# Optimization experiments

Measured on AMD Instinct MI355X. Metric: run time of the kernel, lower is better.

Reference implementation:

```python
import jax, jax.numpy as jnp
import numpy as np

N_Q = 10           # qubits
N_BLOCKS = 10      # encoding blocks (== N_Q so adjoint start-index arithmetic matches source)
DIM = 1 << N_Q     # 1024 state-vector dimension
P = 128            # number of data points -> P*P pairwise circuit evaluations

SQRT2 = np.float32(np.sqrt(2.0))

# bits[d, q] = q-th bit (MSB-first) of basis index d
_bits_np = ((np.arange(DIM)[:, None] >> (N_Q - 1 - np.arange(N_Q))) & 1).astype(np.float32)
BITS = jnp.asarray(_bits_np)  # [DIM, N_Q]
# CRZ-ring diagonal feature: control q, target (q+1) % N_Q; phase exp(1j*theta_q*s_q*(s_{q+1}-1/2))
RING = jnp.asarray(_bits_np * (np.roll(_bits_np, -1, axis=1) - 0.5))  # [DIM, N_Q]


def _apply_1q(state, U, q):
    # state: [B, DIM]; apply 2x2 U to qubit q (MSB-first ordering)
    B = state.shape[0]
    s = state.reshape(B, 1 << q, 2, 1 << (N_Q - q - 1))
    s = jnp.einsum('ij,bajc->baic', U, s)
    return s.reshape(B, DIM)


def h_layer(state):
    H = jnp.asarray([[1, 1], [1, -1]], dtype=state.dtype) / SQRT2
    for q in range(N_Q):
        state = _apply_1q(state, H, q)
    return state


def rz_layer(state, thetas):
    # thetas: [B, N_Q] per-pair data angles; RZ(t) = diag(e^{-it/2}, e^{it/2})
    phases = jnp.exp(1j * jnp.einsum('dq,bq->bd', BITS - 0.5, thetas))
    return state * phases.astype(state.dtype)


def ry_layer(state, thetas):
    # thetas: [N_Q] shared trainable angles
    for q in range(N_Q):
        c, s = jnp.cos(thetas[q] / 2), jnp.sin(thetas[q] / 2)
        U = jnp.stack([jnp.stack([c, -s]), jnp.stack([s, c])]).astype(state.dtype)
        state = _apply_1q(state, U, q)
    return state


def crz_ring(state, thetas):
    # entire CRZ ring is diagonal in the computational basis -> single fused multiply
    phases = jnp.exp(1j * (RING @ thetas))  # [DIM]
    return state * phases.astype(state.dtype)


def circuit(x1, x2, params):
    # x1, x2: [B, N_BLOCKS*N_Q]; params: [N_BLOCKS, 2, N_Q]
    B = x1.shape[0]
    state = jnp.zeros((B, DIM), jnp.complex64).at[:, 0].set(1.0)
    for j in range(N_BLOCKS):  # block(...)
        state = h_layer(state)
        state = rz_layer(state, x1[:, j * N_Q:(j + 1) * N_Q])
        state = ry_layer(state, params[j, 0])
        state = crz_ring(state, params[j, 1])
    for k in range(N_BLOCKS):  # adj_block(...) over reversed(params)
        bp = params[N_BLOCKS - 1 - k]
        start = (N_Q - k - 1) * N_Q  # exactly as written in the source
        state = crz_ring(state, -bp[1])   # adjoint of diagonal gate = negated angles
        state = ry_layer(state, -bp[0])   # RY(-t); single-qubit gates commute across qubits
        state = rz_layer(state, -x2[:, start:start + N_Q])
        state = h_layer(state)            # H is self-adjoint
    return state


def setup_inputs() -> dict:
    key = jax.random.key(0)
    k1, k2, k3 = jax.random.split(key, 3)
    data = jax.random.normal(k1, (P, N_BLOCKS * N_Q), jnp.float32)
    labels = jnp.sign(jax.random.normal(k2, (P,), jnp.float32))  # +/-1 class labels
    params = jax.random.normal(k3, (N_BLOCKS, 2, N_Q), jnp.float32)
    return {"data": data, "labels": labels, "params": params}


def reference(data, labels, params):
    # k_fusion: kernel-target-alignment over all (i, j) pairs, fully batched
    n = data.shape[0]
    x1 = jnp.repeat(data, n, axis=0)   # point i for each pair (pair-major)
    x2 = jnp.tile(data, (n, 1))        # point j for each pair
    state = circuit(x1, x2, params)
    K = (jnp.abs(state[:, 0]) ** 2).reshape(n, n)  # probability of |0...0>
    ll = labels[:, None] * labels[None, :]
    polarity = jnp.sum(ll * K)
    norm = jnp.sqrt(jnp.sum(K ** 2) * jnp.sum(ll ** 2))
    return polarity / norm
```

## Files before the change

kernel.cpp:

```cpp
#include <hip/hip_runtime.h>
#include <math.h>

#define NQ   10
#define DIM  1024
#define NB   10
#define NPTS 128
#define S2   0.70710678118654752440f

#define TS 32
#define KC 64
#define KSPLIT (DIM / KC)
#define NBLK_RED 64

typedef float f2 __attribute__((ext_vector_type(2)));

__device__ __forceinline__ f2 cmul(f2 a, f2 b) {
    return (f2){a.x * b.x - a.y * b.y, a.x * b.y + a.y * b.x};
}

__global__ __launch_bounds__(256)
void states_kernel(const float* __restrict__ data,
                   const float* __restrict__ params,
                   float2* __restrict__ psi,
                   double* __restrict__ acc,
                   int* __restrict__ cnt)
{
    __shared__ f2    Tb[2][16 * 64];
    __shared__ f2    UT[NB * NQ * 4];
    __shared__ float sCrz[NB * NQ];

    const int tid  = threadIdx.x;
    const int w    = tid >> 6;
    const int lane = tid & 63;
    const int pt   = blockIdx.x;

    if (pt == 0 && tid == 0) { acc[0] = 0.0; acc[1] = 0.0; cnt[0] = 0; }

    if (tid < NB * NQ) {
        const int j = tid / NQ, q = tid - j * NQ;
        const float th = params[j * 2 * NQ + q];
        float c, s;
        __sincosf(0.5f * th, &s, &c);
        const float x = data[pt * (NB * NQ) + tid];
        float cx, sx;
        __sincosf(0.5f * x, &sx, &cx);
        const float al = (c - s) * S2, be = (c + s) * S2;
        f2* u = &UT[tid * 4];
        u[0] = (f2){ al * cx, -be * sx};
        u[1] = (f2){ be * cx, -al * sx};
        u[2] = (f2){ be * cx,  al * sx};
        u[3] = (f2){-al * cx, -be * sx};
        sCrz[tid] = params[j * 2 * NQ + NQ + q];
    }
    __syncthreads();

    f2 v[4];
    #pragma unroll
    for (int m = 0; m < 4; ++m) v[m] = (f2){0.f, 0.f};
    if (tid == 0) v[0] = (f2){1.f, 0.f};

    const float B2 = (float)( lane       & 1), B3 = (float)((lane >> 1) & 1);
    const float B4 = (float)((lane >> 2) & 1), B5 = (float)((lane >> 3) & 1);
    const float B6 = (float)((lane >> 4) & 1), B7 = (float)((lane >> 5) & 1);

    #define LOAD_U(j, q) \
        const f2* _u = &UT[((j) * NQ + (q)) * 4]; \
        const f2 u0 = _u[0], u1 = _u[1], u2 = _u[2], u3 = _u[3];

    #define APPLY_LOCAL(j, q, bit) { \
        LOAD_U(j, q) \
        _Pragma("unroll") \
        for (int m = 0; m < 4; ++m) if (!(m & (bit))) { \
            const f2 a0 = v[m], a1 = v[m | (bit)]; \
            v[m]         = cmul(u0, a0) + cmul(u1, a1); \
            v[m | (bit)] = cmul(u2, a0) + cmul(u3, a1); \
        } }

    #define APPLY_SHUFFLE(j, q, mb) { \
        LOAD_U(j, q) \
        const bool hi = lane & (mb); \
        const f2 cv = hi ? u3 : u0; \
        const f2 cp = hi ? u2 : u1; \
        _Pragma("unroll") \
        for (int m = 0; m < 4; ++m) { \
            const f2 p = { __shfl_xor(v[m].x, (mb), 64), \
                           __shfl_xor(v[m].y, (mb), 64) }; \
            v[m] = cmul(cv, v[m]) + cmul(cp, p); \
        } }

    #define TRANSPOSE(buf) { \
        f2* T = Tb[buf]; \
        _Pragma("unroll") \
        for (int m = 0; m < 4; ++m) T[(w * 4 + m) * 64 + lane] = v[m]; \
        __syncthreads(); \
        f2 nv0 = T[(0 * 4 + w) * 64 + lane]; \
        f2 nv1 = T[(1 * 4 + w) * 64 + lane]; \
        f2 nv2 = T[(2 * 4 + w) * 64 + lane]; \
        f2 nv3 = T[(3 * 4 + w) * 64 + lane]; \
        v[0] = nv0; v[1] = nv1; v[2] = nv2; v[3] = nv3; }

    #define APPLY_CRZ(j, hiIsAmp) { \
        const float* phi = &sCrz[(j) * NQ]; \
        const float laneOnly = phi[2] * B7 * (B6 - 0.5f) \
                             + phi[3] * B6 * (B5 - 0.5f) \
                             + phi[4] * B5 * (B4 - 0.5f) \
                             + phi[5] * B4 * (B3 - 0.5f) \
                             + phi[6] * B3 * (B2 - 0.5f); \
        _Pragma("unroll") \
        for (int m = 0; m < 4; ++m) { \
            const int hi2 = (hiIsAmp) ? m : w; \
            const int lo2 = (hiIsAmp) ? w : m; \
            const float b9 = (float)((hi2 >> 1) & 1), b8 = (float)(hi2 & 1); \
            const float b1 = (float)((lo2 >> 1) & 1), b0 = (float)(lo2 & 1); \
            const float ph = laneOnly \
                           + phi[0] * b9 * (b8 - 0.5f) \
                           + phi[1] * b8 * (B7 - 0.5f) \
                           + phi[7] * B2 * (b1 - 0.5f) \
                           + phi[8] * b1 * (b0 - 0.5f) \
                           + phi[9] * b0 * (b9 - 0.5f); \
            float sc, cc; \
            __sincosf(ph, &sc, &cc); \
            v[m] = cmul(v[m], (f2){cc, sc}); \
        } }

    #pragma unroll
    for (int jj = 0; jj < NB / 2; ++jj) {
        const int je = 2 * jj;
        APPLY_LOCAL(je, 9, 1)
        APPLY_LOCAL(je, 8, 2)
        APPLY_SHUFFLE(je, 7, 1)
        APPLY_SHUFFLE(je, 6, 2)
        APPLY_SHUFFLE(je, 5, 4)
        APPLY_SHUFFLE(je, 4, 8)
        APPLY_SHUFFLE(je, 3, 16)
        APPLY_SHUFFLE(je, 2, 32)
        TRANSPOSE(0)
        APPLY_LOCAL(je, 1, 1)
        APPLY_LOCAL(je, 0, 2)
        APPLY_CRZ(je, true)

        const int jo = je + 1;
        APPLY_LOCAL(jo, 1, 1)
        APPLY_LOCAL(jo, 0, 2)
        APPLY_SHUFFLE(jo, 7, 1)
        APPLY_SHUFFLE(jo, 6, 2)
        APPLY_SHUFFLE(jo, 5, 4)
        APPLY_SHUFFLE(jo, 4, 8)
        APPLY_SHUFFLE(jo, 3, 16)
        APPLY_SHUFFLE(jo, 2, 32)
        TRANSPOSE(1)
        APPLY_LOCAL(jo, 9, 1)
        APPLY_LOCAL(jo, 8, 2)
        APPLY_CRZ(jo, false)
    }

    float2* o = psi + (size_t)pt * DIM + w * 256 + lane * 4;
    *(float4*)&o[0] = make_float4(v[0].x, v[0].y, v[1].x, v[1].y);
    *(float4*)&o[2] = make_float4(v[2].x, v[2].y, v[3].x, v[3].y);
}

__global__ __launch_bounds__(256)
void gram_kernel(const float2* __restrict__ psi, float2* __restrict__ Gpart)
{
    __shared__ float2 A [TS][KC + 2];
    __shared__ float2 Bt[KC][TS + 2];

    const int tid  = threadIdx.x;
    const int bx   = blockIdx.x;
    const int ks   = bx & 15;
    const int tile = bx >> 4;
    const int ti   = tile >> 2, tj = tile & 3;
    const int kbase = ks * KC;

    #pragma unroll
    for (int it = 0; it < 2; ++it) {
        const int slot = it * 256 + tid;
        const int row  = slot >> 4;
        const int kq   = (slot & 15) << 2;
        const float4* sa = (const float4*)(psi + (ti * TS + row) * DIM + kbase + kq);
        const float4 a01 = sa[0], a23 = sa[1];
        *(float4*)&A[row][kq]     = a01;
        *(float4*)&A[row][kq + 2] = a23;
        const float4* sb = (const float4*)(psi + (tj * TS + row) * DIM + kbase + kq);
        const float4 b01 = sb[0], b23 = sb[1];
        Bt[kq + 0][row] = make_float2(b01.x, b01.y);
        Bt[kq + 1][row] = make_float2(b01.z, b01.w);
        Bt[kq + 2][row] = make_float2(b23.x, b23.y);
        Bt[kq + 3][row] = make_float2(b23.z, b23.w);
    }
    __syncthreads();

    const int ty = tid >> 4, tx = tid & 15;
    float g00r = 0.f, g00i = 0.f, g01r = 0.f, g01i = 0.f;
    float g10r = 0.f, g10i = 0.f, g11r = 0.f, g11i = 0.f;

    #pragma unroll 4
    for (int k = 0; k < KC; k += 2) {
        const float4 a0 = *(const float4*)&A[2 * ty    ][k];
        const float4 a1 = *(const float4*)&A[2 * ty + 1][k];
        const float4 b0 = *(const float4*)&Bt[k    ][2 * tx];
        const float4 b1 = *(const float4*)&Bt[k + 1][2 * tx];
        g00r += a0.x * b0.x + a0.y * b0.y;  g00i += a0.x * b0.y - a0.y * b0.x;
        g01r += a0.x * b0.z + a0.y * b0.w;  g01i += a0.x * b0.w - a0.y * b0.z;
        g10r += a1.x * b0.x + a1.y * b0.y;  g10i += a1.x * b0.y - a1.y * b0.x;
        g11r += a1.x * b0.z + a1.y * b0.w;  g11i += a1.x * b0.w - a1.y * b0.z;
        g00r += a0.z * b1.x + a0.w * b1.y;  g00i += a0.z * b1.y - a0.w * b1.x;
        g01r += a0.z * b1.z + a0.w * b1.w;  g01i += a0.z * b1.w - a0.w * b1.z;
        g10r += a1.z * b1.x + a1.w * b1.y;  g10i += a1.z * b1.y - a1.w * b1.x;
        g11r += a1.z * b1.z + a1.w * b1.w;  g11i += a1.z * b1.w - a1.w * b1.z;
    }

    float2* gp = Gpart + ks * (NPTS * NPTS);
    const int gr0 = ti * TS + 2 * ty, gc0 = tj * TS + 2 * tx;
    gp[(gr0    ) * NPTS + gc0    ] = make_float2(g00r, g00i);
    gp[(gr0    ) * NPTS + gc0 + 1] = make_float2(g01r, g01i);
    gp[(gr0 + 1) * NPTS + gc0    ] = make_float2(g10r, g10i);
    gp[(gr0 + 1) * NPTS + gc0 + 1] = make_float2(g11r, g11i);
}

__global__ __launch_bounds__(256)
void reduce_final(const float2* __restrict__ Gpart,
                  const float* __restrict__ labels,
                  double* __restrict__ acc,
                  int* __restrict__ cnt,
                  float* __restrict__ out)
{
    const int idx = blockIdx.x * 256 + threadIdx.x;
    float gr = 0.f, gi = 0.f;
    #pragma unroll
    for (int p = 0; p < KSPLIT; ++p) {
        const float2 g = Gpart[p * (NPTS * NPTS) + idx];
        gr += g.x; gi += g.y;
    }
    const int i  = idx >> 7;
    const int jj = idx & (NPTS - 1);
    const float K = gr * gr + gi * gi;
    double pol = (double)(labels[i] * labels[jj]) * (double)K;
    double k2  = (double)K * (double)K;
    #pragma unroll
    for (int off = 1; off < 64; off <<= 1) {
        pol += __shfl_xor(pol, off, 64);
        k2  += __shfl_xor(k2,  off, 64);
    }
    __shared__ double sp[4], sk[4];
    const int wv = threadIdx.x >> 6;
    if ((threadIdx.x & 63) == 0) { sp[wv] = pol; sk[wv] = k2; }
    __syncthreads();
    if (threadIdx.x == 0) {
        atomicAdd(&acc[0], sp[0] + sp[1] + sp[2] + sp[3]);
        atomicAdd(&acc[1], sk[0] + sk[1] + sk[2] + sk[3]);
        __threadfence();
        const int done = atomicAdd(cnt, 1);
        if (done == NBLK_RED - 1) {
            const double p  = atomicAdd(&acc[0], 0.0);
            const double s2 = atomicAdd(&acc[1], 0.0);
            double sumL2 = 0.0;
            for (int t = 0; t < NPTS; ++t) {
                const double l = (double)labels[t];
                sumL2 += l * l;
            }
            out[0] = (float)(p / (sumL2 * sqrt(s2)));
        }
    }
}

extern "C" void kernel_launch(void* const* d_in, const int* in_sizes, int n_in,
                              void* d_out, int out_size, void* d_ws, size_t ws_size,
                              hipStream_t stream)
{
    const float* data   = (const float*)d_in[0];
    const float* labels = (const float*)d_in[1];
    const float* params = (const float*)d_in[2];
    float* out = (float*)d_out;

    float2* psi   = (float2*)d_ws;
    float2* Gpart = (float2*)((char*)d_ws + (size_t)(1u << 20));
    double* acc   = (double*)((char*)d_ws + (size_t)(3u << 20));
    int*    cnt   = (int*)   ((char*)d_ws + (size_t)(3u << 20) + 16);

    states_kernel<<<NPTS, 256, 0, stream>>>(data, params, psi, acc, cnt);
    gram_kernel<<<256, 256, 0, stream>>>(psi, Gpart);
    reduce_final<<<NBLK_RED, 256, 0, stream>>>(Gpart, labels, acc, cnt, out);
}
```

Before: 88.42 us.

## Fuse qubit-pair gates into 4x4 tables and precompute CRZ phase tables

Combines pairs of single-qubit gates into 4x4 Kronecker matrices, which halves the number of local and shuffle gate passes. Each shuffle pass now does three xor-shuffles per amplitude. CRZ phases are split into a lane-only table and a register/warp table, both computed once per block in shared memory with sincos, so the inner loop no longer evaluates sincos. The first block starts from an analytic product state, which skips applying gates to the basis vector. In exchange it adds shared-memory table setup, more shuffles per pass and more shared-memory reads per gate.

Measured after the change: 87.68 us. About the same (-0.8%).

```diff
diff --git a/kernel.cpp b/kernel.cpp
--- a/kernel.cpp
+++ b/kernel.cpp
@@ -27,6 +27,10 @@
 {
     __shared__ f2    Tb[2][16 * 64];
     __shared__ f2    UT[NB * NQ * 4];
+    __shared__ f2    Kt[NB * 2 * 16];
+    __shared__ f2    Ct[NB * 3 * 16];
+    __shared__ f2    Gt[NB * 64];
+    __shared__ f2    Lt[NB * 64];
     __shared__ float sCrz[NB * NQ];
 
     const int tid  = threadIdx.x;
@@ -38,12 +42,10 @@
 
     if (tid < NB * NQ) {
         const int j = tid / NQ, q = tid - j * NQ;
-        const float th = params[j * 2 * NQ + q];
         float c, s;
-        __sincosf(0.5f * th, &s, &c);
-        const float x = data[pt * (NB * NQ) + tid];
+        __sincosf(0.5f * params[j * 2 * NQ + q], &s, &c);
         float cx, sx;
-        __sincosf(0.5f * x, &sx, &cx);
+        __sincosf(0.5f * data[pt * (NB * NQ) + tid], &sx, &cx);
         const float al = (c - s) * S2, be = (c + s) * S2;
         f2* u = &UT[tid * 4];
         u[0] = (f2){ al * cx, -be * sx};
@@ -54,38 +56,77 @@
     }
     __syncthreads();
 
-    f2 v[4];
-    #pragma unroll
-    for (int m = 0; m < 4; ++m) v[m] = (f2){0.f, 0.f};
-    if (tid == 0) v[0] = (f2){1.f, 0.f};
-
-    const float B2 = (float)( lane       & 1), B3 = (float)((lane >> 1) & 1);
-    const float B4 = (float)((lane >> 2) & 1), B5 = (float)((lane >> 3) & 1);
-    const float B6 = (float)((lane >> 4) & 1), B7 = (float)((lane >> 5) & 1);
-
-    #define LOAD_U(j, q) \
-        const f2* _u = &UT[((j) * NQ + (q)) * 4]; \
-        const f2 u0 = _u[0], u1 = _u[1], u2 = _u[2], u3 = _u[3];
-
-    #define APPLY_LOCAL(j, q, bit) { \
-        LOAD_U(j, q) \
-        _Pragma("unroll") \
-        for (int m = 0; m < 4; ++m) if (!(m & (bit))) { \
-            const f2 a0 = v[m], a1 = v[m | (bit)]; \
-            v[m]         = cmul(u0, a0) + cmul(u1, a1); \
-            v[m | (bit)] = cmul(u2, a0) + cmul(u3, a1); \
-        } }
-
-    #define APPLY_SHUFFLE(j, q, mb) { \
-        LOAD_U(j, q) \
-        const bool hi = lane & (mb); \
-        const f2 cv = hi ? u3 : u0; \
-        const f2 cp = hi ? u2 : u1; \
+    for (int e = tid; e < NB * 2 * 16; e += 256) {
+        const int j = e >> 5, side = (e >> 4) & 1, a = (e >> 2) & 3, b = e & 3;
+        const int qh = side ? 0 : 8, ql = side ? 1 : 9;
+        Kt[e] = cmul(UT[(j * NQ + qh) * 4 + ((a >> 1) * 2 + (b >> 1))],
+                     UT[(j * NQ + ql) * 4 + ((a & 1) * 2 + (b & 1))]);
+    }
+    for (int e = tid; e < NB * 3 * 16; e += 256) {
+        const int j = e / 48, r = e - j * 48;
+        const int p = r >> 4, k = r & 15, combo = k >> 2, t = k & 3;
+        const int la = combo & 1, lb = (combo >> 1) & 1;
+        const int ta = t & 1, tb = (t >> 1) & 1;
+        const int qa = 7 - 2 * p, qb = 6 - 2 * p;
+        Ct[e] = cmul(UT[(j * NQ + qa) * 4 + (la * 2 + (la ^ ta))],
+                     UT[(j * NQ + qb) * 4 + (lb * 2 + (lb ^ tb))]);
+    }
+    for (int e = tid; e < NB * 64; e += 256) {
+        const int j = e >> 6, r = e & 63;
+        const float m1 = (float)((r >> 5) & 1), m0 = (float)((r >> 4) & 1);
+        const float w1 = (float)((r >> 3) & 1), w0 = (float)((r >> 2) & 1);
+        const float b7 = (float)((r >> 1) & 1), b2 = (float)(r & 1);
+        const float* phi = &sCrz[j * NQ];
+        float g;
+        if ((j & 1) == 0)
+            g = phi[0] * m1 * (m0 - 0.5f) + phi[1] * m0 * (b7 - 0.5f)
+              + phi[7] * b2 * (w1 - 0.5f) + phi[8] * w1 * (w0 - 0.5f)
+              + phi[9] * w0 * (m1 - 0.5f);
+        else
+            g = phi[0] * w1 * (w0 - 0.5f) + phi[1] * w0 * (b7 - 0.5f)
+              + phi[7] * b2 * (m1 - 0.5f) + phi[8] * m1 * (m0 - 0.5f)
+              + phi[9] * m0 * (w1 - 0.5f);
+        float s, c;
+        __sincosf(g, &s, &c);
+        Gt[e] = (f2){c, s};
+    }
+    for (int e = tid; e < NB * 64; e += 256) {
+        const int j = e >> 6, ln = e & 63;
+        const float B2 = (float)( ln       & 1), B3 = (float)((ln >> 1) & 1);
+        const float B4 = (float)((ln >> 2) & 1), B5 = (float)((ln >> 3) & 1);
+        const float B6 = (float)((ln >> 4) & 1), B7 = (float)((ln >> 5) & 1);
+        const float* phi = &sCrz[j * NQ];
+        const float lo = phi[2] * B7 * (B6 - 0.5f) + phi[3] * B6 * (B5 - 0.5f)
+                       + phi[4] * B5 * (B4 - 0.5f) + phi[5] * B4 * (B3 - 0.5f)
+                       + phi[6] * B3 * (B2 - 0.5f);
+        float s, c;
+        __sincosf(lo, &s, &c);
+        Lt[e] = (f2){c, s};
+    }
+    __syncthreads();
+
+    const int b72 = ((((lane >> 5) & 1)) << 1) | (lane & 1);
+
+    #define LOCAL4(j, side) { \
+        const f2* Km = &Kt[((j) * 2 + (side)) * 16]; \
+        f2 n0 = cmul(Km[ 0], v[0]) + cmul(Km[ 1], v[1]) + cmul(Km[ 2], v[2]) + cmul(Km[ 3], v[3]); \
+        f2 n1 = cmul(Km[ 4], v[0]) + cmul(Km[ 5], v[1]) + cmul(Km[ 6], v[2]) + cmul(Km[ 7], v[3]); \
+        f2 n2 = cmul(Km[ 8], v[0]) + cmul(Km[ 9], v[1]) + cmul(Km[10], v[2]) + cmul(Km[11], v[3]); \
+        f2 n3 = cmul(Km[12], v[0]) + cmul(Km[13], v[1]) + cmul(Km[14], v[2]) + cmul(Km[15], v[3]); \
+        v[0] = n0; v[1] = n1; v[2] = n2; v[3] = n3; }
+
+    #define SHUF4(j, p) { \
+        const int sh = 2 * (p); \
+        const int combo = (((lane >> (sh + 1)) & 1) << 1) | ((lane >> sh) & 1); \
+        const f2* Cm = &Ct[((j) * 3 + (p)) * 16 + combo * 4]; \
+        const f2 c0 = Cm[0], c1 = Cm[1], c2 = Cm[2], c3 = Cm[3]; \
         _Pragma("unroll") \
         for (int m = 0; m < 4; ++m) { \
-            const f2 p = { __shfl_xor(v[m].x, (mb), 64), \
-                           __shfl_xor(v[m].y, (mb), 64) }; \
-            v[m] = cmul(cv, v[m]) + cmul(cp, p); \
+            const f2 x = v[m]; \
+            const f2 p1 = { __shfl_xor(x.x, 1 << sh, 64), __shfl_xor(x.y, 1 << sh, 64) }; \
+            const f2 p2 = { __shfl_xor(x.x, 2 << sh, 64), __shfl_xor(x.y, 2 << sh, 64) }; \
+            const f2 p3 = { __shfl_xor(x.x, 3 << sh, 64), __shfl_xor(x.y, 3 << sh, 64) }; \
+            v[m] = cmul(c0, x) + cmul(c1, p1) + cmul(c2, p2) + cmul(c3, p3); \
         } }
 
     #define TRANSPOSE(buf) { \
@@ -99,59 +140,44 @@
         f2 nv3 = T[(3 * 4 + w) * 64 + lane]; \
         v[0] = nv0; v[1] = nv1; v[2] = nv2; v[3] = nv3; }
 
-    #define APPLY_CRZ(j, hiIsAmp) { \
-        const float* phi = &sCrz[(j) * NQ]; \
-        const float laneOnly = phi[2] * B7 * (B6 - 0.5f) \
-                             + phi[3] * B6 * (B5 - 0.5f) \
-                             + phi[4] * B5 * (B4 - 0.5f) \
-                             + phi[5] * B4 * (B3 - 0.5f) \
-                             + phi[6] * B3 * (B2 - 0.5f); \
+    #define CRZ4(j) { \
+        const f2 l = Lt[((j) << 6) | lane]; \
         _Pragma("unroll") \
         for (int m = 0; m < 4; ++m) { \
-            const int hi2 = (hiIsAmp) ? m : w; \
-            const int lo2 = (hiIsAmp) ? w : m; \
-            const float b9 = (float)((hi2 >> 1) & 1), b8 = (float)(hi2 & 1); \
-            const float b1 = (float)((lo2 >> 1) & 1), b0 = (float)(lo2 & 1); \
-            const float ph = laneOnly \
-                           + phi[0] * b9 * (b8 - 0.5f) \
-                           + phi[1] * b8 * (B7 - 0.5f) \
-                           + phi[7] * B2 * (b1 - 0.5f) \
-                           + phi[8] * b1 * (b0 - 0.5f) \
-                           + phi[9] * b0 * (b9 - 0.5f); \
-            float sc, cc; \
-            __sincosf(ph, &sc, &cc); \
-            v[m] = cmul(v[m], (f2){cc, sc}); \
+            const f2 g = Gt[((j) << 6) | (m << 4) | (w << 2) | b72]; \
+            v[m] = cmul(v[m], cmul(l, g)); \
         } }
 
+    f2 v[4];
+    {
+        f2 f = UT[2 * 4 + ((lane >> 5) & 1) * 2];
+        #pragma unroll
+        for (int q = 3; q <= 7; ++q)
+            f = cmul(f, UT[q * 4 + ((lane >> (7 - q)) & 1) * 2]);
+        f = cmul(f, UT[8 * 4 + ((w >> 1) & 1) * 2]);
+        f = cmul(f, UT[9 * 4 + (w & 1) * 2]);
+        #pragma unroll
+        for (int m = 0; m < 4; ++m)
+            v[m] = cmul(cmul(UT[0 * 4 + ((m >> 1) & 1) * 2],
+                             UT[1 * 4 + (m & 1) * 2]), f);
+    }
+    CRZ4(0)
+
     #pragma unroll
-    for (int jj = 0; jj < NB / 2; ++jj) {
-        const int je = 2 * jj;
-        APPLY_LOCAL(je, 9, 1)
-        APPLY_LOCAL(je, 8, 2)
-        APPLY_SHUFFLE(je, 7, 1)
-        APPLY_SHUFFLE(je, 6, 2)
-        APPLY_SHUFFLE(je, 5, 4)
-        APPLY_SHUFFLE(je, 4, 8)
-        APPLY_SHUFFLE(je, 3, 16)
-        APPLY_SHUFFLE(je, 2, 32)
-        TRANSPOSE(0)
-        APPLY_LOCAL(je, 1, 1)
-        APPLY_LOCAL(je, 0, 2)
-        APPLY_CRZ(je, true)
-
-        const int jo = je + 1;
-        APPLY_LOCAL(jo, 1, 1)
-        APPLY_LOCAL(jo, 0, 2)
-        APPLY_SHUFFLE(jo, 7, 1)
-        APPLY_SHUFFLE(jo, 6, 2)
-        APPLY_SHUFFLE(jo, 5, 4)
-        APPLY_SHUFFLE(jo, 4, 8)
-        APPLY_SHUFFLE(jo, 3, 16)
-        APPLY_SHUFFLE(jo, 2, 32)
-        TRANSPOSE(1)
-        APPLY_LOCAL(jo, 9, 1)
-        APPLY_LOCAL(jo, 8, 2)
-        APPLY_CRZ(jo, false)
+    for (int j = 1; j < NB; ++j) {
+        if (j & 1) {
+            LOCAL4(j, 1)
+            SHUF4(j, 0) SHUF4(j, 1) SHUF4(j, 2)
+            TRANSPOSE(j & 1)
+            LOCAL4(j, 0)
+            CRZ4(j)
+        } else {
+            LOCAL4(j, 0)
+            SHUF4(j, 0) SHUF4(j, 1) SHUF4(j, 2)
+            TRANSPOSE(j & 1)
+            LOCAL4(j, 1)
+            CRZ4(j)
+        }
     }
 
     float2* o = psi + (size_t)pt * DIM + w * 256 + lane * 4;
```

## Run state simulation with one wavefront per point and shared-memory transposes

Applied to the files above, without the earlier changes.

The states kernel now uses a single 64-lane wavefront per data point, with each lane holding 16 amplitudes. Gates are applied in registers and qubit remapping goes through padded LDS transposes instead of cross-lane shuffles and block-wide barriers. The first block's state is built directly as a product state, and the CRZ phases are precomputed as separable lane and register tables, so the inner loop needs no sincos. The trade-off is higher register pressure and only 128 wavefronts across the whole GPU. The transposes also rely on single-wavefront execution without explicit barriers.

Result: slower. 106.3 us (+20.2%).

```diff
diff --git a/kernel.cpp b/kernel.cpp
--- a/kernel.cpp
+++ b/kernel.cpp
@@ -18,145 +18,145 @@
     return (f2){a.x * b.x - a.y * b.y, a.x * b.y + a.y * b.x};
 }
 
-__global__ __launch_bounds__(256)
+__global__ __launch_bounds__(64)
 void states_kernel(const float* __restrict__ data,
                    const float* __restrict__ params,
                    float2* __restrict__ psi,
                    double* __restrict__ acc,
                    int* __restrict__ cnt)
 {
-    __shared__ f2    Tb[2][16 * 64];
+    __shared__ f2    T[16 * 65];
     __shared__ f2    UT[NB * NQ * 4];
+    __shared__ f2    Lt[NB * 64];
+    __shared__ f2    Gt[NB * 64];
     __shared__ float sCrz[NB * NQ];
 
-    const int tid  = threadIdx.x;
-    const int w    = tid >> 6;
-    const int lane = tid & 63;
+    const int lane = threadIdx.x;
     const int pt   = blockIdx.x;
 
-    if (pt == 0 && tid == 0) { acc[0] = 0.0; acc[1] = 0.0; cnt[0] = 0; }
-
-    if (tid < NB * NQ) {
-        const int j = tid / NQ, q = tid - j * NQ;
-        const float th = params[j * 2 * NQ + q];
+    if (pt == 0 && lane == 0) { acc[0] = 0.0; acc[1] = 0.0; cnt[0] = 0; }
+
+    for (int e = lane; e < NB * NQ; e += 64) {
+        const int j = e / NQ, q = e - j * NQ;
         float c, s;
-        __sincosf(0.5f * th, &s, &c);
-        const float x = data[pt * (NB * NQ) + tid];
+        __sincosf(0.5f * params[j * 2 * NQ + q], &s, &c);
         float cx, sx;
-        __sincosf(0.5f * x, &sx, &cx);
+        __sincosf(0.5f * data[pt * (NB * NQ) + e], &sx, &cx);
         const float al = (c - s) * S2, be = (c + s) * S2;
-        f2* u = &UT[tid * 4];
+        f2* u = &UT[e * 4];
         u[0] = (f2){ al * cx, -be * sx};
         u[1] = (f2){ be * cx, -al * sx};
         u[2] = (f2){ be * cx,  al * sx};
         u[3] = (f2){-al * cx, -be * sx};
-        sCrz[tid] = params[j * 2 * NQ + NQ + q];
-    }
-    __syncthreads();
-
-    f2 v[4];
-    #pragma unroll
-    for (int m = 0; m < 4; ++m) v[m] = (f2){0.f, 0.f};
-    if (tid == 0) v[0] = (f2){1.f, 0.f};
-
-    const float B2 = (float)( lane       & 1), B3 = (float)((lane >> 1) & 1);
-    const float B4 = (float)((lane >> 2) & 1), B5 = (float)((lane >> 3) & 1);
-    const float B6 = (float)((lane >> 4) & 1), B7 = (float)((lane >> 5) & 1);
-
-    #define LOAD_U(j, q) \
+        sCrz[e] = params[j * 2 * NQ + NQ + q];
+    }
+    for (int e = lane; e < NB * 64; e += 64) {
+        const int j = e >> 6, r = e & 63;
+        const float* phi = &sCrz[j * NQ];
+        const float r0 = (float)(r & 1),        r1 = (float)((r >> 1) & 1);
+        const float r2 = (float)((r >> 2) & 1), r3 = (float)((r >> 3) & 1);
+        const float r4 = (float)((r >> 4) & 1), r5 = (float)((r >> 5) & 1);
+        const float m0 = r2, m1 = r3, m2 = r4, m3 = r5;
+        const float bA = r1, bB = r0;
+        float L, G;
+        if ((j & 1) == 0) {
+            L = phi[4] * r5 * (r4 - 0.5f) + phi[5] * r4 * (r3 - 0.5f)
+              + phi[6] * r3 * (r2 - 0.5f) + phi[7] * r2 * (r1 - 0.5f)
+              + phi[8] * r1 * (r0 - 0.5f);
+            G = phi[0] * m3 * (m2 - 0.5f) + phi[1] * m2 * (m1 - 0.5f)
+              + phi[2] * m1 * (m0 - 0.5f) + phi[3] * m0 * (bA - 0.5f)
+              + phi[9] * bB * (m3 - 0.5f);
+        } else {
+            L = phi[0] * r5 * (r4 - 0.5f) + phi[1] * r4 * (r3 - 0.5f)
+              + phi[2] * r3 * (r2 - 0.5f) + phi[3] * r2 * (r1 - 0.5f)
+              + phi[4] * r1 * (r0 - 0.5f);
+            G = phi[6] * m3 * (m2 - 0.5f) + phi[7] * m2 * (m1 - 0.5f)
+              + phi[8] * m1 * (m0 - 0.5f) + phi[5] * bA * (m3 - 0.5f)
+              + phi[9] * m0 * (bB - 0.5f);
+        }
+        float s, c;
+        __sincosf(L, &s, &c);  Lt[e] = (f2){c, s};
+        __sincosf(G, &s, &c);  Gt[e] = (f2){c, s};
+    }
+
+    #define APPLY(j, q, bit) { \
         const f2* _u = &UT[((j) * NQ + (q)) * 4]; \
-        const f2 u0 = _u[0], u1 = _u[1], u2 = _u[2], u3 = _u[3];
-
-    #define APPLY_LOCAL(j, q, bit) { \
-        LOAD_U(j, q) \
-        _Pragma("unroll") \
-        for (int m = 0; m < 4; ++m) if (!(m & (bit))) { \
+        const f2 u0 = _u[0], u1 = _u[1], u2 = _u[2], u3 = _u[3]; \
+        _Pragma("unroll") \
+        for (int m = 0; m < 16; ++m) if (!(m & (bit))) { \
             const f2 a0 = v[m], a1 = v[m | (bit)]; \
             v[m]         = cmul(u0, a0) + cmul(u1, a1); \
             v[m | (bit)] = cmul(u2, a0) + cmul(u3, a1); \
         } }
 
-    #define APPLY_SHUFFLE(j, q, mb) { \
-        LOAD_U(j, q) \
-        const bool hi = lane & (mb); \
-        const f2 cv = hi ? u3 : u0; \
-        const f2 cp = hi ? u2 : u1; \
-        _Pragma("unroll") \
-        for (int m = 0; m < 4; ++m) { \
-            const f2 p = { __shfl_xor(v[m].x, (mb), 64), \
-                           __shfl_xor(v[m].y, (mb), 64) }; \
-            v[m] = cmul(cv, v[m]) + cmul(cp, p); \
+    #define TWRITE() { \
+        _Pragma("unroll") \
+        for (int m = 0; m < 16; ++m) T[m * 65 + lane] = v[m]; }
+
+    #define READ_AD() { \
+        const int base = 65 * (lane & 15) + ((lane >> 4) << 4); \
+        _Pragma("unroll") \
+        for (int m = 0; m < 16; ++m) v[m] = T[base + m]; }
+
+    #define READ_B() { \
+        _Pragma("unroll") \
+        for (int m = 0; m < 16; ++m) \
+            v[m] = T[65 * (((m & 3) << 2) | (lane >> 4)) + ((m >> 2) << 4) + (lane & 15)]; }
+
+    #define READ_C() { \
+        _Pragma("unroll") \
+        for (int m = 0; m < 16; ++m) \
+            v[m] = T[65 * (((lane >> 4) << 2) | (m >> 2)) + ((m & 3) << 4) + (lane & 15)]; }
+
+    #define CRZ(j, crossIdx) { \
+        const f2 l = Lt[((j) << 6) | lane]; \
+        _Pragma("unroll") \
+        for (int m = 0; m < 16; ++m) { \
+            const f2 g = Gt[((j) << 6) | (m << 2) | (crossIdx)]; \
+            v[m] = cmul(v[m], cmul(l, g)); \
         } }
 
-    #define TRANSPOSE(buf) { \
-        f2* T = Tb[buf]; \
-        _Pragma("unroll") \
-        for (int m = 0; m < 4; ++m) T[(w * 4 + m) * 64 + lane] = v[m]; \
-        __syncthreads(); \
-        f2 nv0 = T[(0 * 4 + w) * 64 + lane]; \
-        f2 nv1 = T[(1 * 4 + w) * 64 + lane]; \
-        f2 nv2 = T[(2 * 4 + w) * 64 + lane]; \
-        f2 nv3 = T[(3 * 4 + w) * 64 + lane]; \
-        v[0] = nv0; v[1] = nv1; v[2] = nv2; v[3] = nv3; }
-
-    #define APPLY_CRZ(j, hiIsAmp) { \
-        const float* phi = &sCrz[(j) * NQ]; \
-        const float laneOnly = phi[2] * B7 * (B6 - 0.5f) \
-                             + phi[3] * B6 * (B5 - 0.5f) \
-                             + phi[4] * B5 * (B4 - 0.5f) \
-                             + phi[5] * B4 * (B3 - 0.5f) \
-                             + phi[6] * B3 * (B2 - 0.5f); \
-        _Pragma("unroll") \
-        for (int m = 0; m < 4; ++m) { \
-            const int hi2 = (hiIsAmp) ? m : w; \
-            const int lo2 = (hiIsAmp) ? w : m; \
-            const float b9 = (float)((hi2 >> 1) & 1), b8 = (float)(hi2 & 1); \
-            const float b1 = (float)((lo2 >> 1) & 1), b0 = (float)(lo2 & 1); \
-            const float ph = laneOnly \
-                           + phi[0] * b9 * (b8 - 0.5f) \
-                           + phi[1] * b8 * (B7 - 0.5f) \
-                           + phi[7] * B2 * (b1 - 0.5f) \
-                           + phi[8] * b1 * (b0 - 0.5f) \
-                           + phi[9] * b0 * (b9 - 0.5f); \
-            float sc, cc; \
-            __sincosf(ph, &sc, &cc); \
-            v[m] = cmul(v[m], (f2){cc, sc}); \
-        } }
-
-    #pragma unroll
-    for (int jj = 0; jj < NB / 2; ++jj) {
-        const int je = 2 * jj;
-        APPLY_LOCAL(je, 9, 1)
-        APPLY_LOCAL(je, 8, 2)
-        APPLY_SHUFFLE(je, 7, 1)
-        APPLY_SHUFFLE(je, 6, 2)
-        APPLY_SHUFFLE(je, 5, 4)
-        APPLY_SHUFFLE(je, 4, 8)
-        APPLY_SHUFFLE(je, 3, 16)
-        APPLY_SHUFFLE(je, 2, 32)
-        TRANSPOSE(0)
-        APPLY_LOCAL(je, 1, 1)
-        APPLY_LOCAL(je, 0, 2)
-        APPLY_CRZ(je, true)
-
-        const int jo = je + 1;
-        APPLY_LOCAL(jo, 1, 1)
-        APPLY_LOCAL(jo, 0, 2)
-        APPLY_SHUFFLE(jo, 7, 1)
-        APPLY_SHUFFLE(jo, 6, 2)
-        APPLY_SHUFFLE(jo, 5, 4)
-        APPLY_SHUFFLE(jo, 4, 8)
-        APPLY_SHUFFLE(jo, 3, 16)
-        APPLY_SHUFFLE(jo, 2, 32)
-        TRANSPOSE(1)
-        APPLY_LOCAL(jo, 9, 1)
-        APPLY_LOCAL(jo, 8, 2)
-        APPLY_CRZ(jo, false)
-    }
-
-    float2* o = psi + (size_t)pt * DIM + w * 256 + lane * 4;
-    *(float4*)&o[0] = make_float4(v[0].x, v[0].y, v[1].x, v[1].y);
-    *(float4*)&o[2] = make_float4(v[2].x, v[2].y, v[3].x, v[3].y);
+    f2 v[16];
+    {
+        f2 f = cmul(UT[9 * 4 + (lane & 1) * 2],        UT[8 * 4 + ((lane >> 1) & 1) * 2]);
+        f = cmul(f, cmul(UT[7 * 4 + ((lane >> 2) & 1) * 2], UT[6 * 4 + ((lane >> 3) & 1) * 2]));
+        f = cmul(f, cmul(UT[5 * 4 + ((lane >> 4) & 1) * 2], UT[4 * 4 + ((lane >> 5) & 1) * 2]));
+        #pragma unroll
+        for (int m = 0; m < 16; ++m) {
+            const f2 rm = cmul(cmul(UT[0 * 4 + ((m >> 3) & 1) * 2],
+                                    UT[1 * 4 + ((m >> 2) & 1) * 2]),
+                               cmul(UT[2 * 4 + ((m >> 1) & 1) * 2],
+                                    UT[3 * 4 + (m & 1) * 2]));
+            v[m] = cmul(rm, f);
+        }
+    }
+    const int crossEven = (((lane >> 5) & 1) << 1) | (lane & 1);
+    const int crossOdd  = ((lane & 1) << 1) | ((lane >> 5) & 1);
+    CRZ(0, crossEven)
+
+    #pragma unroll 1
+    for (int j = 1; j < NB; ++j) {
+        if (j & 1) {
+            APPLY(j, 0, 8) APPLY(j, 1, 4) APPLY(j, 2, 2) APPLY(j, 3, 1)
+            TWRITE() READ_C()
+            APPLY(j, 4, 2) APPLY(j, 5, 1)
+            TWRITE() READ_AD()
+            APPLY(j, 6, 8) APPLY(j, 7, 4) APPLY(j, 8, 2) APPLY(j, 9, 1)
+            CRZ(j, crossOdd)
+        } else {
+            APPLY(j, 6, 8) APPLY(j, 7, 4) APPLY(j, 8, 2) APPLY(j, 9, 1)
+            TWRITE() READ_AD()
+            APPLY(j, 2, 8) APPLY(j, 3, 4) APPLY(j, 4, 2) APPLY(j, 5, 1)
+            TWRITE() READ_B()
+            APPLY(j, 0, 8) APPLY(j, 1, 4)
+            CRZ(j, crossEven)
+        }
+    }
+
+    float2* o = psi + (size_t)pt * DIM + lane * 16;
+    #pragma unroll
+    for (int k = 0; k < 8; ++k)
+        *(float4*)&o[2 * k] = make_float4(v[2*k].x, v[2*k].y, v[2*k+1].x, v[2*k+1].y);
 }
 
 __global__ __launch_bounds__(256)
@@ -278,7 +278,7 @@
     double* acc   = (double*)((char*)d_ws + (size_t)(3u << 20));
     int*    cnt   = (int*)   ((char*)d_ws + (size_t)(3u << 20) + 16);
 
-    states_kernel<<<NPTS, 256, 0, stream>>>(data, params, psi, acc, cnt);
+    states_kernel<<<NPTS, 64, 0, stream>>>(data, params, psi, acc, cnt);
     gram_kernel<<<256, 256, 0, stream>>>(psi, Gpart);
-    reduce_final<<<NBLK_RED, 256, 0, stream>>>(Gpart, labels, acc, cnt, out);
-}
+    reduce_final<<<NBLK_RED, 64 * 4, 0, stream>>>(Gpart, labels, acc, cnt, out);
+}
```
